# Optimization experiments

Measured on AMD Instinct MI355X. Metric: run time of the kernel, lower is better.

Reference implementation:

```python
import jax, jax.numpy as jnp
import numpy as np

H = W = 128
SCALE = 4
Q = (SCALE * H) * (SCALE * W)
C = 64
E = 4


def _conv2d(x, w, b, pad):
    y = jax.lax.conv_general_dilated(x, w, (1, 1), [(pad, pad), (pad, pad)],
                                     dimension_numbers=('NCHW', 'OIHW', 'NCHW'))
    return y + b[None, :, None, None]


def _conv1x1(x, w, b):
    return jnp.einsum('oc,bchw->bohw', w, x) + b[None, :, None, None]


def _bilinear_zeros(img, gx, gy):
    # img: [C,Hs,Ws]; gx,gy: [Hh,Wh] normalized coords, align_corners=True, zeros padding
    c, Hs, Ws = img.shape
    x = (gx + 1.0) * 0.5 * (Ws - 1)
    y = (gy + 1.0) * 0.5 * (Hs - 1)
    x0 = jnp.floor(x)
    y0 = jnp.floor(y)
    wx1 = x - x0; wx0 = 1.0 - wx1
    wy1 = y - y0; wy0 = 1.0 - wy1
    x0i = x0.astype(jnp.int32); y0i = y0.astype(jnp.int32)

    def gather(yi, xi):
        m = ((xi >= 0) & (xi < Ws) & (yi >= 0) & (yi < Hs)).astype(img.dtype)
        v = img[:, jnp.clip(yi, 0, Hs - 1), jnp.clip(xi, 0, Ws - 1)]
        return v * m  # [C,Hh,Wh]

    return (gather(y0i, x0i) * (wy0 * wx0) + gather(y0i, x0i + 1) * (wy0 * wx1)
            + gather(y0i + 1, x0i) * (wy1 * wx0) + gather(y0i + 1, x0i + 1) * (wy1 * wx1))


def setup_inputs() -> dict:
    key = jax.random.key(0)
    ks = jax.random.split(key, 18)
    s = 0.1
    d = {}
    d['inp'] = jax.random.normal(ks[0], (1, 3, H, W), jnp.float32)
    d['coord'] = jax.random.uniform(ks[1], (1, Q, 2), jnp.float32, -1.0, 1.0)
    d['cell'] = jnp.full((1, Q, 2), 2.0 / (SCALE * H), jnp.float32)  # cell = 2/(scale*h) exactly
    d['enc_w'] = jax.random.normal(ks[2], (C, 3, 3, 3), jnp.float32) * s
    d['enc_b'] = jax.random.normal(ks[3], (C,), jnp.float32) * s
    d['body_w1'] = jax.random.normal(ks[4], (C, 4), jnp.float32) * s
    d['body_b1'] = jax.random.normal(ks[5], (C,), jnp.float32) * s
    d['body_w2'] = jax.random.normal(ks[6], (C, C), jnp.float32) * s
    d['body_b2'] = jax.random.normal(ks[7], (C,), jnp.float32) * s
    d['routing_w'] = jax.random.normal(ks[8], (E, C), jnp.float32) * s
    d['routing_b'] = jax.random.normal(ks[9], (E,), jnp.float32) * s
    d['offset_w'] = jax.random.normal(ks[10], (2, C), jnp.float32) * s
    d['offset_b'] = jax.random.normal(ks[11], (2,), jnp.float32) * s
    d['tail_w'] = jax.random.normal(ks[12], (3, C, 3, 3), jnp.float32) * s
    d['tail_b'] = jax.random.normal(ks[13], (3,), jnp.float32) * s
    d['weight_compress'] = jax.random.normal(ks[14], (E, C // 8, C), jnp.float32) * s
    d['weight_expand'] = jax.random.normal(ks[15], (E, C, C // 8), jnp.float32) * s
    d['scale'] = SCALE
    return d


def reference(inp, coord, cell, enc_w, enc_b, body_w1, body_b1, body_w2, body_b2,
              routing_w, routing_b, offset_w, offset_b, tail_w, tail_b,
              weight_compress, weight_expand, scale):
    feat = _conv2d(inp, enc_w, enc_b, pad=1)        # encoder -> [1,64,h,w]
    _, c, h, w = feat.shape
    Hh, Wh = scale * h, scale * w
    fs = float(scale)

    # scale embedding input: [1/scale, 1/scale, coor_h, coor_w]
    ih = jnp.arange(Hh, dtype=jnp.float32)
    iw = jnp.arange(Wh, dtype=jnp.float32)
    coor_h = (ih + 0.5) / fs - jnp.floor((ih + 0.5) / fs + 0.001) - 0.5
    coor_w = (iw + 0.5) / fs - jnp.floor((iw + 0.5) / fs + 0.001) - 0.5
    cs = jnp.full((Hh, Wh), 1.0 / fs, jnp.float32)
    inp4 = jnp.stack([cs, cs,
                      jnp.broadcast_to(coor_h[:, None], (Hh, Wh)),
                      jnp.broadcast_to(coor_w[None, :], (Hh, Wh))])[None]  # [1,4,Hh,Wh]

    emb = jax.nn.relu(_conv1x1(inp4, body_w1, body_b1))
    emb = jax.nn.relu(_conv1x1(emb, body_w2, body_b2))
    off = _conv1x1(emb, offset_w, offset_b)[0]                 # [2,Hh,Wh]
    r = jax.nn.sigmoid(_conv1x1(emb, routing_w, routing_b))[0]  # [E,Hh,Wh]

    # offset grid_sample of LR feat onto HR grid (align_corners=True, zeros pad)
    xx, yy = jnp.meshgrid(jnp.arange(Wh, dtype=jnp.float32), jnp.arange(Hh, dtype=jnp.float32))
    gx = (((xx + 0.5) / fs - 0.5) * 2.0 / (w - 1) - 1.0) + off[0] * 2.0 / (w - 1)
    gy = (((yy + 0.5) / fs - 0.5) * 2.0 / (h - 1) - 1.0) + off[1] * 2.0 / (h - 1)
    fea0 = _bilinear_zeros(feat[0], gx, gy)                    # [c,Hh,Wh]

    # per-pixel expert mixing; linear in routing, so apply experts then mix
    t = jnp.einsum('ekc,chw->ekhw', weight_compress, fea0)     # [E,c/8,Hh,Wh]
    mid = jnp.einsum('ehw,ekhw->khw', r, t)                    # [c/8,Hh,Wh]
    u = jnp.einsum('eck,khw->echw', weight_expand, mid)        # [E,c,Hh,Wh]
    out2 = jnp.einsum('ehw,echw->chw', r, u)                   # [c,Hh,Wh]

    pred = _conv2d((out2 + fea0)[None], tail_w, tail_b, pad=1)[0]  # [3,Hh,Wh]

    # nearest-neighbour query (align_corners=True)
    coord_q = jnp.clip(coord - cell * 0.5 + 1e-6, -1.0 + 1e-6, 1.0 - 1e-6)[0]  # [Q,2] (y,x)
    gxq = coord_q[:, 1]
    gyq = coord_q[:, 0]
    xi = jnp.clip(jnp.round((gxq + 1.0) * 0.5 * (Wh - 1)).astype(jnp.int32), 0, Wh - 1)
    yi = jnp.clip(jnp.round((gyq + 1.0) * 0.5 * (Hh - 1)).astype(jnp.int32), 0, Hh - 1)
    q = pred[:, yi, xi].T                                      # [Q,3]
    return q[None]                                             # [1,Q,3]
```

## Files before the change

kernel.cpp:

```cpp
#include <hip/hip_runtime.h>
#include <hip/hip_bf16.h>

typedef __hip_bfloat16 bf16;
typedef __fp16 h2 __attribute__((ext_vector_type(2)));

__device__ __forceinline__ float bf2f(bf16 h) { return __bfloat162float(h); }
__device__ __forceinline__ bf16 us2bf(unsigned short u){ union{unsigned short s; bf16 h;}v; v.s=u; return v.h; }
__device__ __forceinline__ float asf(unsigned u){ union{unsigned u; float f;}v; v.u=u; return v.f; }
__device__ __forceinline__ h2 uh(unsigned u){ union{unsigned u; h2 h;}v; v.u=u; return v.h; }
__device__ __forceinline__ unsigned pkh(float a, float b){ union{h2 h; unsigned u;}v; v.h=__builtin_amdgcn_cvt_pkrtz(a,b); return v.u; }
__device__ __forceinline__ unsigned short f2bu(float a){ union{bf16 h; unsigned short u;}v; v.h=__float2bfloat16(a); return v.u; }
__device__ __forceinline__ unsigned pkbf(float a, float b){ return ((unsigned)f2bu(b) << 16) | (unsigned)f2bu(a); }
#define FDOT2(va,vb,acc) __builtin_amdgcn_fdot2((va),(vb),(acc),false)

#define HH 128
#define WW 128
#define HS 512
#define WSZ 512
#define QN (HS*WSZ)

#define O_OFFTAB 0
#define O_TB     32
#define O_TW2    64
#define O_CWC2   1024
#define O_W2P    5120
#define O_FEAT   8192
#define O_PRED   1056768

#define SH_W2T 0
#define SH_WE  4160
#define SH_WC  6208
#define SH_TW  8256
#define SH_OW  9984
#define SH_RW  10112
#define SH_END 10368

__constant__ int PREF2[16] = {0,15,27,39,54,64,72,80,90,100,108,116,126,141,153,165};

__device__ __forceinline__ float rdin(const void* p, int i, bool f32m) {
  return f32m ? ((const float*)p)[i] : bf2f(((const bf16*)p)[i]);
}
__device__ __forceinline__ float rdw(const void* p, int i, bool f32m) {
  if (f32m) return ((const float*)p)[i];
  unsigned u = ((const unsigned*)p)[i>>1];
  return asf((i&1) ? (u & 0xffff0000u) : (u<<16));
}
__device__ __forceinline__ bool sniff_f32(const void* inp) {
  int lane = threadIdx.x & 63;
  unsigned short u = ((const unsigned short*)inp)[2*lane];
  float v = bf2f(us2bf(u));
  bool ok = (v == v) && (fabsf(v) < 64.0f);
  return __popcll(__ballot(ok)) < 48;
}
__device__ __forceinline__ unsigned blend4(unsigned a, unsigned b, unsigned c, unsigned d,
                                           h2 W00, h2 W01, h2 W10, h2 W11) {
  h2 f = uh(a)*W00 + uh(b)*W01 + uh(c)*W10 + uh(d)*W11;
  union{h2 h; unsigned u;} v; v.h = f; return v.u;
}

__global__ __launch_bounds__(256) void k_prep(
    const void* __restrict__ inp, const void* __restrict__ encw, const void* __restrict__ encb,
    const void* __restrict__ w1, const void* __restrict__ b1,
    const void* __restrict__ w2, const void* __restrict__ b2,
    const void* __restrict__ rw, const void* __restrict__ rb,
    const void* __restrict__ ow, const void* __restrict__ ob,
    const void* __restrict__ tw, const void* __restrict__ tb,
    const void* __restrict__ wc, const void* __restrict__ we,
    float* __restrict__ ws) {
  __shared__ float shpool[SH_END];
  __shared__ float sh1[64];
  __shared__ float sh2[64];
  __shared__ float shr[4];
  __shared__ float shcwe[512];
  bool f32m = sniff_f32(inp);
  int b = blockIdx.x, t = threadIdx.x;
  unsigned* wsu = (unsigned*)ws;

  if (b < 256) {
    int g = b >> 6;
    int px = (b & 63)*256 + t;
    float* shw = shpool;
    float* shb = shpool + 432;
    for (int i = t; i < 432; i += 256) shw[i] = rdw(encw, g*432 + i, f32m);
    if (t < 16) shb[t] = rdw(encb, g*16 + t, f32m);
    __syncthreads();
    int x = px & 127, y = px >> 7;
    float tp[27];
    #pragma unroll
    for (int ic = 0; ic < 3; ic++)
      #pragma unroll
      for (int dy = 0; dy < 3; dy++) {
        int yy = y + dy - 1;
        #pragma unroll
        for (int dx = 0; dx < 3; dx++) {
          int xx = x + dx - 1;
          bool ok = (yy >= 0) & (yy < 128) & (xx >= 0) & (xx < 128);
          tp[ic*9 + dy*3 + dx] = ok ? rdin(inp, ic*16384 + yy*128 + xx, f32m) : 0.0f;
        }
      }
    unsigned e[8];
    #pragma unroll
    for (int o4 = 0; o4 < 4; o4++) {
      float a[4];
      #pragma unroll
      for (int oo = 0; oo < 4; oo++) {
        int o2 = o4*4 + oo;
        float acc = shb[o2];
        #pragma unroll
        for (int kk = 0; kk < 27; kk++) acc = fmaf(shw[o2*27 + kk], tp[kk], acc);
        a[oo] = acc;
      }
      e[o4*2]   = pkh(a[0], a[1]);
      e[o4*2+1] = pkh(a[2], a[3]);
    }
    uint4* outp = (uint4*)(wsu + O_FEAT + px*32 + g*8);
    outp[0] = make_uint4(e[0], e[1], e[2], e[3]);
    outp[1] = make_uint4(e[4], e[5], e[6], e[7]);
  } else if (b < 272) {
    int cls = b - 256;
    for (int i = t; i < 4096; i += 256) shpool[SH_W2T + (i & 63)*65 + (i >> 6)] = rdw(w2, i, f32m);
    for (int i = t; i < 2048; i += 256) { shpool[SH_WE + i] = rdw(we, i, f32m); shpool[SH_WC + i] = rdw(wc, i, f32m); }
    for (int i = t; i < 1728; i += 256) shpool[SH_TW + i] = rdw(tw, i, f32m);
    for (int i = t; i < 128; i += 256)  shpool[SH_OW + i] = rdw(ow, i, f32m);
    for (int i = t; i < 256; i += 256)  shpool[SH_RW + i] = rdw(rw, i, f32m);
    if (t < 64) {
      float mcls = (float)(cls >> 2), ncls = (float)(cls & 3);
      float chv = (mcls + 0.5f)*0.25f - 0.5f;
      float cwv = (ncls + 0.5f)*0.25f - 0.5f;
      float s1 = rdw(w1,t*4+0,f32m)*0.25f + rdw(w1,t*4+1,f32m)*0.25f
               + rdw(w1,t*4+2,f32m)*chv + rdw(w1,t*4+3,f32m)*cwv + rdw(b1,t,f32m);
      sh1[t] = fmaxf(s1, 0.0f);
    }
    __syncthreads();
    if (t < 64) {
      float s2 = rdw(b2,t,f32m);
      for (int i = 0; i < 64; i++) s2 = fmaf(shpool[SH_W2T + i*65 + t], sh1[i], s2);
      sh2[t] = fmaxf(s2, 0.0f);
    }
    __syncthreads();
    if (t < 2) {
      float a = rdw(ob,t,f32m);
      for (int i = 0; i < 64; i++) a = fmaf(shpool[SH_OW + t*64 + i], sh2[i], a);
      ws[O_OFFTAB + cls*2 + t] = a;
    } else if (t < 6) {
      int e = t - 2;
      float a = rdw(rb,e,f32m);
      for (int i = 0; i < 64; i++) a = fmaf(shpool[SH_RW + e*64 + i], sh2[i], a);
      shr[e] = 1.0f / (1.0f + expf(-a));
    }
    __syncthreads();
    float r0 = shr[0], r1 = shr[1], r2 = shr[2], r3 = shr[3];
    for (int idx = t; idx < 512; idx += 256) {
      float a =       r0 * shpool[SH_WE + idx];
      a = fmaf(r1, shpool[SH_WE +  512 + idx], a);
      a = fmaf(r2, shpool[SH_WE + 1024 + idx], a);
      a = fmaf(r3, shpool[SH_WE + 1536 + idx], a);
      shcwe[idx] = a;
    }
    unsigned* wcw = wsu + O_CWC2 + cls*256;
    for (int idx = t; idx < 256; idx += 256) {
      int cp = idx >> 3, k = idx & 7;
      float lo =       r0 * shpool[SH_WC +        k*64 + 2*cp];
      lo = fmaf(r1, shpool[SH_WC +  512 + k*64 + 2*cp], lo);
      lo = fmaf(r2, shpool[SH_WC + 1024 + k*64 + 2*cp], lo);
      lo = fmaf(r3, shpool[SH_WC + 1536 + k*64 + 2*cp], lo);
      float hi =       r0 * shpool[SH_WC +        k*64 + 2*cp + 1];
      hi = fmaf(r1, shpool[SH_WC +  512 + k*64 + 2*cp + 1], hi);
      hi = fmaf(r2, shpool[SH_WC + 1024 + k*64 + 2*cp + 1], hi);
      hi = fmaf(r3, shpool[SH_WC + 1536 + k*64 + 2*cp + 1], hi);
      wcw[idx] = pkh(lo, hi);
    }
    __syncthreads();
    unsigned* wpp = wsu + O_W2P;
    for (int idx = t; idx < 108; idx += 256) {
      int j = idx / 12, rem = idx - j*12, o2 = rem >> 2, kp = rem & 3;
      float alo = 0.0f, ahi = 0.0f;
      for (int c = 0; c < 64; c++) {
        float tv = shpool[SH_TW + (o2*64 + c)*9 + j];
        alo = fmaf(tv, shcwe[c*8 + 2*kp],     alo);
        ahi = fmaf(tv, shcwe[c*8 + 2*kp + 1], ahi);
      }
      wpp[(cls*9 + j)*12 + o2*4 + kp] = pkh(alo, ahi);
    }
  } else {
    for (int idx = t; idx < 864; idx += 256) {
      int o2 = idx / 288, rem = idx - o2*288, j = rem >> 5, cp = rem & 31;
      unsigned d = pkh(rdw(tw, (o2*64 + 2*cp    )*9 + j, f32m),
                       rdw(tw, (o2*64 + 2*cp + 1)*9 + j, f32m));
      (wsu + O_TW2)[idx] = d;
    }
    if (t < 3) ws[O_TB + t] = rdin(tb, t, f32m);
  }
}

__global__ __launch_bounds__(512) void k_maintail(const float* __restrict__ ws, unsigned* __restrict__ pred4) {
  __shared__ unsigned shf[32*181];
  __shared__ __align__(16) unsigned shm4[181*4];
  __shared__ unsigned short scls[192];
  __shared__ float spart[3*384];
  const unsigned* wsu = (const unsigned*)ws;
  int blk = blockIdx.x;
  int xcd = blk & 7, local = blk >> 3;
  int ty0 = (xcd*8 + (local >> 5)) * 8;
  int tx0 = (local & 31) * 16;
  int t = threadIdx.x;
  int q = t & 1;
  const uint4* F2 = (const uint4*)(wsu + O_FEAT);

  int s = t >> 1;
  if (s < 180) {
    int cls = 0;
    #pragma unroll
    for (int i = 1; i < 16; i++) cls += (s >= PREF2[i]) ? 1 : 0;
    int j = s - PREF2[cls];
    int a = cls >> 2, bb = cls & 3;
    int nx = ((bb == 0) | (bb == 3)) ? 5 : 4;
    int jy = (nx == 4) ? (j >> 2) : ((j*13) >> 6);
    int jx = j - jy*nx;
    int py = ((a + 1) & 3) + 4*jy;
    int px = ((bb + 1) & 3) + 4*jx;
    int pos = py*18 + px;
    int gy = ty0 - 1 + py, gx = tx0 - 1 + px;
    if ((gy < 0) | (gy >= HS) | (gx < 0) | (gx >= WSZ)) {
      if (q == 0) scls[pos] = 0;
      #pragma unroll
      for (int i = 0; i < 16; i++) shf[(q*16 + i)*181 + pos] = 0u;
      shm4[pos*4 + q*2 + 0] = 0u;
      shm4[pos*4 + q*2 + 1] = 0u;
    } else {
      if (q == 0) scls[pos] = (unsigned short)cls;
      float off0 = ws[O_OFFTAB + cls*2 + 0];
      float off1 = ws[O_OFFTAB + cls*2 + 1];
      float gxf = (((float)gx + 0.5f)*0.25f - 0.5f)*(2.0f/127.0f) - 1.0f + off0*(2.0f/127.0f);
      float gyf = (((float)gy + 0.5f)*0.25f - 0.5f)*(2.0f/127.0f) - 1.0f + off1*(2.0f/127.0f);
      float sx = (gxf + 1.0f)*0.5f*127.0f;
      float sy = (gyf + 1.0f)*0.5f*127.0f;
      float x0f = floorf(sx), y0f = floorf(sy);
      float fx = sx - x0f, fy = sy - y0f;
      int ix0 = (int)x0f, iy0 = (int)y0f;
      int ix1 = ix0 + 1, iy1 = iy0 + 1;
      float wx0 = 1.0f - fx, wy0 = 1.0f - fy;
      float w00 = wy0*wx0, w01 = wy0*fx, w10 = fy*wx0, w11 = fy*fx;
      bool vx0 = (ix0 >= 0) & (ix0 < WW), vx1 = (ix1 >= 0) & (ix1 < WW);
      bool vy0 = (iy0 >= 0) & (iy0 < HH), vy1 = (iy1 >= 0) & (iy1 < HH);
      if (!(vy0 & vx0)) w00 = 0.0f;
      if (!(vy0 & vx1)) w01 = 0.0f;
      if (!(vy1 & vx0)) w10 = 0.0f;
      if (!(vy1 & vx1)) w11 = 0.0f;
      int cx0 = min(max(ix0, 0), WW-1), cx1 = min(max(ix1, 0), WW-1);
      int cy0 = min(max(iy0, 0), HH-1), cy1 = min(max(iy1, 0), HH-1);
      int b00 = (cy0*WW + cx0)*8 + q*4, b01 = (cy0*WW + cx1)*8 + q*4;
      int b10 = (cy1*WW + cx0)*8 + q*4, b11 = (cy1*WW + cx1)*8 + q*4;

      uint4 A0 = F2[b00+0], A1 = F2[b00+1], A2 = F2[b00+2], A3 = F2[b00+3];
      uint4 B0 = F2[b01+0], B1 = F2[b01+1], B2 = F2[b01+2], B3 = F2[b01+3];
      uint4 C0 = F2[b10+0], C1 = F2[b10+1], C2 = F2[b10+2], C3 = F2[b10+3];
      uint4 D0 = F2[b11+0], D1 = F2[b11+1], D2 = F2[b11+2], D3 = F2[b11+3];

      h2 W00 = { (__fp16)w00, (__fp16)w00 };
      h2 W01 = { (__fp16)w01, (__fp16)w01 };
      h2 W10 = { (__fp16)w10, (__fp16)w10 };
      h2 W11 = { (__fp16)w11, (__fp16)w11 };

      unsigned fp[16];
      fp[ 0] = blend4(A0.x,B0.x,C0.x,D0.x,W00,W01,W10,W11);
      fp[ 1] = blend4(A0.y,B0.y,C0.y,D0.y,W00,W01,W10,W11);
      fp[ 2] = blend4(A0.z,B0.z,C0.z,D0.z,W00,W01,W10,W11);
      fp[ 3] = blend4(A0.w,B0.w,C0.w,D0.w,W00,W01,W10,W11);
      fp[ 4] = blend4(A1.x,B1.x,C1.x,D1.x,W00,W01,W10,W11);
      fp[ 5] = blend4(A1.y,B1.y,C1.y,D1.y,W00,W01,W10,W11);
      fp[ 6] = blend4(A1.z,B1.z,C1.z,D1.z,W00,W01,W10,W11);
      fp[ 7] = blend4(A1.w,B1.w,C1.w,D1.w,W00,W01,W10,W11);
      fp[ 8] = blend4(A2.x,B2.x,C2.x,D2.x,W00,W01,W10,W11);
      fp[ 9] = blend4(A2.y,B2.y,C2.y,D2.y,W00,W01,W10,W11);
      fp[10] = blend4(A2.z,B2.z,C2.z,D2.z,W00,W01,W10,W11);
      fp[11] = blend4(A2.w,B2.w,C2.w,D2.w,W00,W01,W10,W11);
      fp[12] = blend4(A3.x,B3.x,C3.x,D3.x,W00,W01,W10,W11);
      fp[13] = blend4(A3.y,B3.y,C3.y,D3.y,W00,W01,W10,W11);
      fp[14] = blend4(A3.z,B3.z,C3.z,D3.z,W00,W01,W10,W11);
      fp[15] = blend4(A3.w,B3.w,C3.w,D3.w,W00,W01,W10,W11);

      #pragma unroll
      for (int i = 0; i < 16; i++) shf[(q*16 + i)*181 + pos] = fp[i];

      const uint4* CWv = (const uint4*)(wsu + O_CWC2 + cls*256) + q*32;
      float mid[8] = {0,0,0,0,0,0,0,0};
      #pragma unroll
      for (int i = 0; i < 16; i++) {
        uint4 w0 = CWv[i*2], w1 = CWv[i*2+1];
        h2 f = uh(fp[i]);
        mid[0] = FDOT2(f, uh(w0.x), mid[0]); mid[1] = FDOT2(f, uh(w0.y), mid[1]);
        mid[2] = FDOT2(f, uh(w0.z), mid[2]); mid[3] = FDOT2(f, uh(w0.w), mid[3]);
        mid[4] = FDOT2(f, uh(w1.x), mid[4]); mid[5] = FDOT2(f, uh(w1.y), mid[5]);
        mid[6] = FDOT2(f, uh(w1.z), mid[6]); mid[7] = FDOT2(f, uh(w1.w), mid[7]);
      }
      #pragma unroll
      for (int k = 0; k < 8; k++) mid[k] += __shfl_xor(mid[k], 1);
      shm4[pos*4 + q*2 + 0] = pkh(mid[q*4+0], mid[q*4+1]);
      shm4[pos*4 + q*2 + 1] = pkh(mid[q*4+2], mid[q*4+3]);
    }
  }
  __syncthreads();

  int split = t >> 7, pi = t & 127;
  int tx = pi & 15, ty = pi >> 4;
  int pos9[9];
  #pragma unroll
  for (int dy = 0; dy < 3; dy++)
    #pragma unroll
    for (int dx = 0; dx < 3; dx++)
      pos9[dy*3 + dx] = (ty + dy)*18 + (tx + dx);
  const unsigned* TW2 = wsu + O_TW2;
  float a0, a1, a2;
  if (split == 0) { a0 = ws[O_TB+0]; a1 = ws[O_TB+1]; a2 = ws[O_TB+2]; }
  else            { a0 = 0.0f; a1 = 0.0f; a2 = 0.0f; }
  int cp0 = split*8;
  for (int cpl = 0; cpl < 8; cpl++) {
    int cp = cp0 + cpl;
    #pragma unroll
    for (int j = 0; j < 9; j++) {
      h2 hv = uh(shf[cp*181 + pos9[j]]);
      a0 = FDOT2(hv, uh(TW2[(0*9 + j)*32 + cp]), a0);
      a1 = FDOT2(hv, uh(TW2[(1*9 + j)*32 + cp]), a1);
      a2 = FDOT2(hv, uh(TW2[(2*9 + j)*32 + cp]), a2);
    }
  }
  {
    const int JB[4] = {0, 2, 5, 7};
    const int JE[4] = {2, 5, 7, 9};
    int jb = JB[split], je = JE[split];
    for (int j = jb; j < je; j++) {
      int pp = pos9[j];
      int cl = scls[pp];
      uint4 mv = *(const uint4*)&shm4[pp*4];
      const uint4* Wp = (const uint4*)(wsu + O_W2P) + (cl*9 + j)*3;
      uint4 w0 = Wp[0], w1 = Wp[1], w2 = Wp[2];
      h2 m0 = uh(mv.x), m1 = uh(mv.y), m2 = uh(mv.z), m3 = uh(mv.w);
      a0 = FDOT2(m0, uh(w0.x), a0); a0 = FDOT2(m1, uh(w0.y), a0);
      a0 = FDOT2(m2, uh(w0.z), a0); a0 = FDOT2(m3, uh(w0.w), a0);
      a1 = FDOT2(m0, uh(w1.x), a1); a1 = FDOT2(m1, uh(w1.y), a1);
      a1 = FDOT2(m2, uh(w1.z), a1); a1 = FDOT2(m3, uh(w1.w), a1);
      a2 = FDOT2(m0, uh(w2.x), a2); a2 = FDOT2(m1, uh(w2.y), a2);
      a2 = FDOT2(m2, uh(w2.z), a2); a2 = FDOT2(m3, uh(w2.w), a2);
    }
  }
  if (split != 0) {
    float* sp = spart + (split-1)*384 + pi*3;
    sp[0] = a0; sp[1] = a1; sp[2] = a2;
  }
  __syncthreads();
  if (split == 0) {
    #pragma unroll
    for (int k = 0; k < 3; k++) {
      const float* sp = spart + k*384 + pi*3;
      a0 += sp[0]; a1 += sp[1]; a2 += sp[2];
    }
    ((uint2*)pred4)[blk*128 + pi] = make_uint2(pkbf(a0, a1), pkbf(a2, 0.0f));
  }
}

__global__ __launch_bounds__(256) void k_gather(const void* __restrict__ inp,
                                                const void* __restrict__ coord, const void* __restrict__ cell,
                                                const float* __restrict__ ws, void* __restrict__ outp) {
  bool f32m = sniff_f32(inp);
  const uint2* pred4 = (const uint2*)((const unsigned*)ws + O_PRED);
  int q = blockIdx.x*256 + threadIdx.x;
  float cy, cx, ly, lx;
  if (f32m) {
    float2 c = ((const float2*)coord)[q]; cy = c.x; cx = c.y;
    float2 l = ((const float2*)cell)[q];  ly = l.x; lx = l.y;
  } else {
    unsigned cu = ((const unsigned*)coord)[q]; cy = asf(cu<<16); cx = asf(cu & 0xffff0000u);
    unsigned lu = ((const unsigned*)cell)[q];  ly = asf(lu<<16); lx = asf(lu & 0xffff0000u);
  }
  float gyq = fminf(fmaxf(cy - ly*0.5f + 1e-6f, -1.0f + 1e-6f), 1.0f - 1e-6f);
  float gxq = fminf(fmaxf(cx - lx*0.5f + 1e-6f, -1.0f + 1e-6f), 1.0f - 1e-6f);
  int xi = (int)rintf((gxq + 1.0f)*0.5f*511.0f);
  int yi = (int)rintf((gyq + 1.0f)*0.5f*511.0f);
  xi = min(max(xi, 0), WSZ-1);
  yi = min(max(yi, 0), HS-1);
  int row = yi >> 3, col = xi >> 4;
  int xcd = row >> 3;
  int local = (row & 7)*32 + col;
  int blk = local*8 + xcd;
  int pi = (yi & 7)*16 + (xi & 15);
  uint2 d = pred4[blk*128 + pi];
  float v0 = asf(d.x << 16), v1 = asf(d.x & 0xffff0000u), v2 = asf(d.y << 16);
  if (f32m) {
    float* o = (float*)outp;
    o[q*3 + 0] = v0; o[q*3 + 1] = v1; o[q*3 + 2] = v2;
  } else {
    bf16* o = (bf16*)outp;
    o[q*3 + 0] = __float2bfloat16(v0);
    o[q*3 + 1] = __float2bfloat16(v1);
    o[q*3 + 2] = __float2bfloat16(v2);
  }
}

extern "C" void kernel_launch(void* const* d_in, const int* in_sizes, int n_in,
                              void* d_out, int out_size, void* d_ws, size_t ws_size,
                              hipStream_t stream) {
  const void* inp   = d_in[0];
  const void* coord = d_in[1];
  const void* cell  = d_in[2];
  const void* encw  = d_in[3];
  const void* encb  = d_in[4];
  const void* w1    = d_in[5];
  const void* b1    = d_in[6];
  const void* w2    = d_in[7];
  const void* b2    = d_in[8];
  const void* rw    = d_in[9];
  const void* rb    = d_in[10];
  const void* ow    = d_in[11];
  const void* ob    = d_in[12];
  const void* tw    = d_in[13];
  const void* tb    = d_in[14];
  const void* wc    = d_in[15];
  const void* we    = d_in[16];

  float* wsf = (float*)d_ws;
  unsigned* pred4 = (unsigned*)wsf + O_PRED;

  k_prep<<<273, 256, 0, stream>>>(inp, encw, encb, w1, b1, w2, b2, rw, rb, ow, ob, tw, tb, wc, we, wsf);
  k_maintail<<<2048, 512, 0, stream>>>(wsf, pred4);
  k_gather<<<1024, 256, 0, stream>>>(inp, coord, cell, wsf, d_out);
}
```

Baseline: 181.5 us.

## Shrink maintail tiles to 8x8 with pixel-major shared layout and vector LDS access

```diff
diff --git a/kernel.cpp b/kernel.cpp
--- a/kernel.cpp
+++ b/kernel.cpp
@@ -17,7 +17,6 @@
 #define WW 128
 #define HS 512
 #define WSZ 512
-#define QN (HS*WSZ)
 
 #define O_OFFTAB 0
 #define O_TB     32
@@ -35,7 +34,7 @@
 #define SH_RW  10112
 #define SH_END 10368
 
-__constant__ int PREF2[16] = {0,15,27,39,54,64,72,80,90,100,108,116,126,141,153,165};
+__constant__ int PREF3[16] = {0,9,15,21,30,36,40,44,50,56,60,64,70,79,85,91};
 
 __device__ __forceinline__ float rdin(const void* p, int i, bool f32m) {
   return f32m ? ((const float*)p)[i] : bf2f(((const bf16*)p)[i]);
@@ -193,40 +192,42 @@
   }
 }
 
-__global__ __launch_bounds__(512) void k_maintail(const float* __restrict__ ws, unsigned* __restrict__ pred4) {
-  __shared__ unsigned shf[32*181];
-  __shared__ __align__(16) unsigned shm4[181*4];
-  __shared__ unsigned short scls[192];
-  __shared__ float spart[3*384];
+__global__ __launch_bounds__(256) void k_maintail(const float* __restrict__ ws, unsigned* __restrict__ pred4) {
+  __shared__ __align__(16) unsigned shd[100*36];
+  __shared__ unsigned short scls[100];
+  __shared__ float spart[3*192];
   const unsigned* wsu = (const unsigned*)ws;
   int blk = blockIdx.x;
   int xcd = blk & 7, local = blk >> 3;
-  int ty0 = (xcd*8 + (local >> 5)) * 8;
-  int tx0 = (local & 31) * 16;
+  int ty0 = (xcd*8 + (local >> 6)) * 8;
+  int tx0 = (local & 63) * 8;
   int t = threadIdx.x;
   int q = t & 1;
   const uint4* F2 = (const uint4*)(wsu + O_FEAT);
 
   int s = t >> 1;
-  if (s < 180) {
+  if (s < 100) {
     int cls = 0;
     #pragma unroll
-    for (int i = 1; i < 16; i++) cls += (s >= PREF2[i]) ? 1 : 0;
-    int j = s - PREF2[cls];
+    for (int i = 1; i < 16; i++) cls += (s >= PREF3[i]) ? 1 : 0;
+    int j = s - PREF3[cls];
     int a = cls >> 2, bb = cls & 3;
-    int nx = ((bb == 0) | (bb == 3)) ? 5 : 4;
-    int jy = (nx == 4) ? (j >> 2) : ((j*13) >> 6);
+    int nx = ((bb == 0) | (bb == 3)) ? 3 : 2;
+    int jy = (nx == 3) ? ((j*11) >> 5) : (j >> 1);
     int jx = j - jy*nx;
     int py = ((a + 1) & 3) + 4*jy;
     int px = ((bb + 1) & 3) + 4*jx;
-    int pos = py*18 + px;
+    int pos = py*10 + px;
+    unsigned* row = &shd[pos*36 + q*16];
     int gy = ty0 - 1 + py, gx = tx0 - 1 + px;
     if ((gy < 0) | (gy >= HS) | (gx < 0) | (gx >= WSZ)) {
       if (q == 0) scls[pos] = 0;
-      #pragma unroll
-      for (int i = 0; i < 16; i++) shf[(q*16 + i)*181 + pos] = 0u;
-      shm4[pos*4 + q*2 + 0] = 0u;
-      shm4[pos*4 + q*2 + 1] = 0u;
+      ((uint4*)row)[0] = make_uint4(0,0,0,0);
+      ((uint4*)row)[1] = make_uint4(0,0,0,0);
+      ((uint4*)row)[2] = make_uint4(0,0,0,0);
+      ((uint4*)row)[3] = make_uint4(0,0,0,0);
+      shd[pos*36 + 32 + q*2 + 0] = 0u;
+      shd[pos*36 + 32 + q*2 + 1] = 0u;
     } else {
       if (q == 0) scls[pos] = (unsigned short)cls;
       float off0 = ws[O_OFFTAB + cls*2 + 0];
@@ -280,8 +281,10 @@
       fp[14] = blend4(A3.z,B3.z,C3.z,D3.z,W00,W01,W10,W11);
       fp[15] = blend4(A3.w,B3.w,C3.w,D3.w,W00,W01,W10,W11);
 
-      #pragma unroll
-      for (int i = 0; i < 16; i++) shf[(q*16 + i)*181 + pos] = fp[i];
+      ((uint4*)row)[0] = make_uint4(fp[0],  fp[1],  fp[2],  fp[3]);
+      ((uint4*)row)[1] = make_uint4(fp[4],  fp[5],  fp[6],  fp[7]);
+      ((uint4*)row)[2] = make_uint4(fp[8],  fp[9],  fp[10], fp[11]);
+      ((uint4*)row)[3] = make_uint4(fp[12], fp[13], fp[14], fp[15]);
 
       const uint4* CWv = (const uint4*)(wsu + O_CWC2 + cls*256) + q*32;
       float mid[8] = {0,0,0,0,0,0,0,0};
@@ -296,43 +299,54 @@
       }
       #pragma unroll
       for (int k = 0; k < 8; k++) mid[k] += __shfl_xor(mid[k], 1);
-      shm4[pos*4 + q*2 + 0] = pkh(mid[q*4+0], mid[q*4+1]);
-      shm4[pos*4 + q*2 + 1] = pkh(mid[q*4+2], mid[q*4+3]);
+      shd[pos*36 + 32 + q*2 + 0] = pkh(mid[q*4+0], mid[q*4+1]);
+      shd[pos*36 + 32 + q*2 + 1] = pkh(mid[q*4+2], mid[q*4+3]);
     }
   }
   __syncthreads();
 
-  int split = t >> 7, pi = t & 127;
-  int tx = pi & 15, ty = pi >> 4;
-  int pos9[9];
-  #pragma unroll
-  for (int dy = 0; dy < 3; dy++)
-    #pragma unroll
-    for (int dx = 0; dx < 3; dx++)
-      pos9[dy*3 + dx] = (ty + dy)*18 + (tx + dx);
+  int split = t >> 6, pi = t & 63;
+  int tx = pi & 7, ty = pi >> 3;
   const unsigned* TW2 = wsu + O_TW2;
   float a0, a1, a2;
   if (split == 0) { a0 = ws[O_TB+0]; a1 = ws[O_TB+1]; a2 = ws[O_TB+2]; }
   else            { a0 = 0.0f; a1 = 0.0f; a2 = 0.0f; }
-  int cp0 = split*8;
-  for (int cpl = 0; cpl < 8; cpl++) {
-    int cp = cp0 + cpl;
-    #pragma unroll
-    for (int j = 0; j < 9; j++) {
-      h2 hv = uh(shf[cp*181 + pos9[j]]);
-      a0 = FDOT2(hv, uh(TW2[(0*9 + j)*32 + cp]), a0);
-      a1 = FDOT2(hv, uh(TW2[(1*9 + j)*32 + cp]), a1);
-      a2 = FDOT2(hv, uh(TW2[(2*9 + j)*32 + cp]), a2);
-    }
-  }
-  {
-    const int JB[4] = {0, 2, 5, 7};
-    const int JE[4] = {2, 5, 7, 9};
-    int jb = JB[split], je = JE[split];
-    for (int j = jb; j < je; j++) {
-      int pp = pos9[j];
+  const int JB[4] = {0, 2, 5, 7};
+  const int JE[4] = {2, 5, 7, 9};
+  #pragma unroll
+  for (int j = 0; j < 9; j++) {
+    int dy = j / 3, dx = j - dy*3;
+    int pp = (ty + dy)*10 + (tx + dx);
+    const uint4* frow = (const uint4*)&shd[pp*36 + split*8];
+    uint4 f0 = frow[0], f1 = frow[1];
+    int cb = split*8;
+    a0 = FDOT2(uh(f0.x), uh(TW2[(0*9+j)*32 + cb+0]), a0);
+    a0 = FDOT2(uh(f0.y), uh(TW2[(0*9+j)*32 + cb+1]), a0);
+    a0 = FDOT2(uh(f0.z), uh(TW2[(0*9+j)*32 + cb+2]), a0);
+    a0 = FDOT2(uh(f0.w), uh(TW2[(0*9+j)*32 + cb+3]), a0);
+    a0 = FDOT2(uh(f1.x), uh(TW2[(0*9+j)*32 + cb+4]), a0);
+    a0 = FDOT2(uh(f1.y), uh(TW2[(0*9+j)*32 + cb+5]), a0);
+    a0 = FDOT2(uh(f1.z), uh(TW2[(0*9+j)*32 + cb+6]), a0);
+    a0 = FDOT2(uh(f1.w), uh(TW2[(0*9+j)*32 + cb+7]), a0);
+    a1 = FDOT2(uh(f0.x), uh(TW2[(1*9+j)*32 + cb+0]), a1);
+    a1 = FDOT2(uh(f0.y), uh(TW2[(1*9+j)*32 + cb+1]), a1);
+    a1 = FDOT2(uh(f0.z), uh(TW2[(1*9+j)*32 + cb+2]), a1);
+    a1 = FDOT2(uh(f0.w), uh(TW2[(1*9+j)*32 + cb+3]), a1);
+    a1 = FDOT2(uh(f1.x), uh(TW2[(1*9+j)*32 + cb+4]), a1);
+    a1 = FDOT2(uh(f1.y), uh(TW2[(1*9+j)*32 + cb+5]), a1);
+    a1 = FDOT2(uh(f1.z), uh(TW2[(1*9+j)*32 + cb+6]), a1);
+    a1 = FDOT2(uh(f1.w), uh(TW2[(1*9+j)*32 + cb+7]), a1);
+    a2 = FDOT2(uh(f0.x), uh(TW2[(2*9+j)*32 + cb+0]), a2);
+    a2 = FDOT2(uh(f0.y), uh(TW2[(2*9+j)*32 + cb+1]), a2);
+    a2 = FDOT2(uh(f0.z), uh(TW2[(2*9+j)*32 + cb+2]), a2);
+    a2 = FDOT2(uh(f0.w), uh(TW2[(2*9+j)*32 + cb+3]), a2);
+    a2 = FDOT2(uh(f1.x), uh(TW2[(2*9+j)*32 + cb+4]), a2);
+    a2 = FDOT2(uh(f1.y), uh(TW2[(2*9+j)*32 + cb+5]), a2);
+    a2 = FDOT2(uh(f1.z), uh(TW2[(2*9+j)*32 + cb+6]), a2);
+    a2 = FDOT2(uh(f1.w), uh(TW2[(2*9+j)*32 + cb+7]), a2);
+    if (j >= JB[split] && j < JE[split]) {
       int cl = scls[pp];
-      uint4 mv = *(const uint4*)&shm4[pp*4];
+      uint4 mv = *(const uint4*)&shd[pp*36 + 32];
       const uint4* Wp = (const uint4*)(wsu + O_W2P) + (cl*9 + j)*3;
       uint4 w0 = Wp[0], w1 = Wp[1], w2 = Wp[2];
       h2 m0 = uh(mv.x), m1 = uh(mv.y), m2 = uh(mv.z), m3 = uh(mv.w);
@@ -345,17 +359,17 @@
     }
   }
   if (split != 0) {
-    float* sp = spart + (split-1)*384 + pi*3;
+    float* sp = spart + (split-1)*192 + pi*3;
     sp[0] = a0; sp[1] = a1; sp[2] = a2;
   }
   __syncthreads();
   if (split == 0) {
     #pragma unroll
     for (int k = 0; k < 3; k++) {
-      const float* sp = spart + k*384 + pi*3;
+      const float* sp = spart + k*192 + pi*3;
       a0 += sp[0]; a1 += sp[1]; a2 += sp[2];
     }
-    ((uint2*)pred4)[blk*128 + pi] = make_uint2(pkbf(a0, a1), pkbf(a2, 0.0f));
+    ((uint2*)pred4)[blk*64 + pi] = make_uint2(pkbf(a0, a1), pkbf(a2, 0.0f));
   }
 }
 
@@ -379,12 +393,12 @@
   int yi = (int)rintf((gyq + 1.0f)*0.5f*511.0f);
   xi = min(max(xi, 0), WSZ-1);
   yi = min(max(yi, 0), HS-1);
-  int row = yi >> 3, col = xi >> 4;
+  int row = yi >> 3, col = xi >> 3;
   int xcd = row >> 3;
-  int local = (row & 7)*32 + col;
+  int local = (row & 7)*64 + col;
   int blk = local*8 + xcd;
-  int pi = (yi & 7)*16 + (xi & 15);
-  uint2 d = pred4[blk*128 + pi];
+  int pi = (yi & 7)*8 + (xi & 7);
+  uint2 d = pred4[blk*64 + pi];
   float v0 = asf(d.x << 16), v1 = asf(d.x & 0xffff0000u), v2 = asf(d.y << 16);
   if (f32m) {
     float* o = (float*)outp;
@@ -422,6 +436,6 @@
   unsigned* pred4 = (unsigned*)wsf + O_PRED;
 
   k_prep<<<273, 256, 0, stream>>>(inp, encw, encb, w1, b1, w2, b2, rw, rb, ow, ob, tw, tb, wc, we, wsf);
-  k_maintail<<<2048, 512, 0, stream>>>(wsf, pred4);
+  k_maintail<<<4096, 256, 0, stream>>>(wsf, pred4);
   k_gather<<<1024, 256, 0, stream>>>(inp, coord, cell, wsf, d_out);
 }
```

Result: no change. 183.2 us (+0.9%).
